# Kernel optimization log

Hardware: AMD Instinct MI355X
Metric: run time of the kernel (lower is better)

## Reference

```python
import jax, jax.numpy as jnp
import numpy as np
import math

# ---- static config (matches init_kwargs) ----
MUL = 16                       # multiplicity of 0e and 1o irreps in/out
IN_DIM = 4 * MUL               # 16x0e + 16x1o -> 16 + 48 = 64 channels
DIAMETER = 7.0
RADIUS = DIAMETER / 2.0
NRB = 8                        # num_radial_basis
STEPS = (1.0, 1.0, 1.0)
N_PATHS = 5                    # 0x0->0, 1x1->0, 0x1->1, 1x0->1, 1x1->1
WEIGHT_NUMEL = N_PATHS * MUL * MUL  # 1280


def _lattice():
    axes = []
    for st in STEPS:
        s = math.floor(RADIUS / st)
        axes.append(np.arange(-s, s + 1.0) * st)
    return np.stack(np.meshgrid(*axes, indexing='ij'), axis=-1).astype(np.float32)  # [kx,ky,kz,3]


def _radial_emb(r):
    # e3nn soft_one_hot_linspace, basis='smooth_finite', cutoff=True
    values = np.linspace(0.0, RADIUS, NRB + 2)[1:-1].astype(np.float32)
    step = values[1] - values[0]
    diff = (r[..., None] - values) / step
    def u(t):  # soft unit step: exp(-1/t) for t>0 else 0
        return np.where(t > 0.0, np.exp(-1.0 / np.where(t > 0.0, t, 1.0)), 0.0)
    return (1.14136 * math.e ** 2 * u(diff + 1.0) * u(1.0 - diff)).astype(np.float32)


def _spherical_harmonics(lat):
    # normalize=True, normalization='component': Y0 = 1, Y1 = sqrt(3) * unit_vec
    n = np.linalg.norm(lat, axis=-1, keepdims=True)
    unit = np.where(n > 0, lat / np.where(n > 0, n, 1.0), 0.0)
    return np.ones(lat.shape[:-1], np.float32), (math.sqrt(3.0) * unit).astype(np.float32)


_LAT = _lattice()
_EMB = jnp.asarray(_radial_emb(np.linalg.norm(_LAT, axis=-1)))  # [kx,ky,kz,NRB]
_sh0_np, _sh1_np = _spherical_harmonics(_LAT)
_SH0, _SH1 = jnp.asarray(_sh0_np), jnp.asarray(_sh1_np)
_eps_np = np.zeros((3, 3, 3), np.float32)
for _i, _j, _k in [(0, 1, 2), (1, 2, 0), (2, 0, 1)]:
    _eps_np[_i, _j, _k] = 1.0
    _eps_np[_i, _k, _j] = -1.0
_EPS = jnp.asarray(_eps_np)


def _build_kernel(tp_weight):
    """Radial-basis matmul + CG tensor-product -> conv kernel [out,in,kx,ky,kz]."""
    kx, ky, kz = _LAT.shape[:3]
    nk = kx * ky * kz
    w = jnp.einsum('xyzb,bn->xyzn', _EMB, tp_weight) / nk
    w = w.reshape(kx, ky, kz, N_PATHS, MUL, MUL)
    w1, w2, w3, w4, w5 = [w[..., p, :, :] for p in range(N_PATHS)]
    # e3nn path weights ('component' norm, 'element' path norm): sqrt(dim_out / fan_in)
    a0 = math.sqrt(1.0 / (2 * MUL))  # -> 0e: paths 1,2 each mul1*mul2 = MUL
    a1 = math.sqrt(3.0 / (3 * MUL))  # -> 1o: paths 3,4,5
    c1 = a0                          # w3j(0,0,0) = 1
    c2 = a0 / math.sqrt(3.0)         # w3j(1,1,0) = delta/sqrt(3)
    c3 = a1 / math.sqrt(3.0)         # w3j(0,1,1) = delta/sqrt(3)
    c4 = a1 / math.sqrt(3.0)         # w3j(1,0,1) = delta/sqrt(3)
    c5 = a1 / math.sqrt(6.0)         # w3j(1,1,1) = eps/sqrt(6)
    Kss = c1 * _SH0[..., None, None] * w1                                  # [k,u,o]
    Kvs = c2 * jnp.einsum('xyzi,xyzuo->xyzuio', _SH1, w2)                  # [k,u,3,o]
    Ksv = c3 * jnp.einsum('xyzk,xyzuo->xyzuok', _SH1, w3)                  # [k,u,o,3]
    eye3 = jnp.eye(3, dtype=w.dtype)
    Kvv = (c4 * jnp.einsum('xyz,ik,xyzuo->xyzuiok', _SH0, eye3, w4)
           + c5 * jnp.einsum('ijk,xyzj,xyzuo->xyzuiok', _EPS, _SH1, w5))   # [k,u,3,o,3]
    top = jnp.concatenate([Kss, Ksv.reshape(kx, ky, kz, MUL, 3 * MUL)], axis=-1)
    bot = jnp.concatenate([Kvs.reshape(kx, ky, kz, 3 * MUL, MUL),
                           Kvv.reshape(kx, ky, kz, 3 * MUL, 3 * MUL)], axis=-1)
    K = jnp.concatenate([top, bot], axis=-2)                               # [kx,ky,kz,in,out]
    return jnp.transpose(K, (4, 3, 0, 1, 2))                               # oixyz


def setup_inputs() -> dict:
    key = jax.random.key(0)
    k1, k2, k3, k4 = jax.random.split(key, 4)
    x = jax.random.normal(k1, (2, IN_DIM, 40, 40, 40), jnp.float32)
    sc_w0 = jax.random.normal(k2, (MUL, MUL), jnp.float32)
    sc_w1 = jax.random.normal(k3, (MUL, MUL), jnp.float32)
    tp_weight = jax.random.normal(k4, (NRB, WEIGHT_NUMEL), jnp.float32)
    return {"x": x, "sc_w0": sc_w0, "sc_w1": sc_w1, "tp_weight": tp_weight}


def reference(x, sc_w0, sc_w1, tp_weight):
    B = x.shape[0]
    sp = x.shape[2:]
    inv = 1.0 / math.sqrt(MUL)  # e3nn Linear fan-in normalization
    x0 = x[:, :MUL]                                  # [B,MUL,D,H,W]
    x1 = x[:, MUL:].reshape(B, MUL, 3, *sp)          # [B,MUL,3,D,H,W]
    sc0 = jnp.einsum('uo,budhw->bodhw', sc_w0, x0) * inv
    sc1 = jnp.einsum('uo,buidhw->boidhw', sc_w1, x1) * inv
    sc = jnp.concatenate([sc0, sc1.reshape(B, 3 * MUL, *sp)], axis=1)
    K = _build_kernel(tp_weight)
    pad = [(s // 2, s // 2) for s in K.shape[2:]]
    conv = jax.lax.conv_general_dilated(
        x, K, window_strides=(1, 1, 1), padding=pad,
        dimension_numbers=('NCDHW', 'OIDHW', 'NCDHW'))
    return sc + conv
```

## Files before the change

### kernel.cpp

```cpp
#include <hip/hip_runtime.h>
#include <stdint.h>


#define NT_REAL 179
#define NT_PAD  180
#define NGRP    45

#define XCH  1557376
#define XCHB ((size_t)XCH * 2)

typedef short s16x8 __attribute__((ext_vector_type(8)));
typedef float f32x4 __attribute__((ext_vector_type(4)));

struct Taps {
  int n;
  short dl16[NT_PAD];
  unsigned char dz[NT_PAD], dy[NT_PAD], dx[NT_PAD];
};
constexpr Taps mk_taps() {
  Taps t{};
  t.n = 0;
  for (int a = 0; a < 7; ++a)
    for (int b = 0; b < 7; ++b)
      for (int c = 0; c < 7; ++c) {
        int d2 = (a-3)*(a-3) + (b-3)*(b-3) + (c-3)*(c-3);
        if (d2 <= 12) {
          t.dz[t.n] = (unsigned char)a; t.dy[t.n] = (unsigned char)b;
          t.dx[t.n] = (unsigned char)c;
          t.dl16[t.n] = (short)((a*14 + b)*16 + c);
          ++t.n;
        }
      }
  for (int i = t.n; i < NT_PAD; ++i) {
    t.dz[i] = 3; t.dy[i] = 3; t.dx[i] = 3; t.dl16[i] = t.dl16[0];
  }
  return t;
}
__device__ constexpr Taps TAPS = mk_taps();
static_assert(mk_taps().n == NT_REAL, "tap count");

struct DL4s { unsigned long long v[NGRP]; };
constexpr DL4s mk_dl4() {
  DL4s d{};
  Taps t = mk_taps();
  for (int g = 0; g < NGRP; ++g) {
    unsigned long long v = 0;
    for (int q = 0; q < 4; ++q)
      v |= (unsigned long long)(unsigned short)t.dl16[g * 4 + q] << (16 * q);
    d.v[g] = v;
  }
  return d;
}
__device__ constexpr DL4s DL4 = mk_dl4();

static __device__ inline unsigned short f2bf(float f) {
  unsigned int u = __float_as_uint(f);
  unsigned int r = u + 0x7FFFu + ((u >> 16) & 1u);
  return (unsigned short)(r >> 16);
}

__device__ __forceinline__ void gl_lds16(const void* g, void* s) {
  __builtin_amdgcn_global_load_lds(
      (const __attribute__((address_space(1))) void*)g,
      (__attribute__((address_space(3))) void*)s, 16, 0, 0);
}

__global__ void prep(const float* __restrict__ x, const float* __restrict__ scw0,
                     const float* __restrict__ scw1, const float* __restrict__ tpw,
                     unsigned short* __restrict__ Xp, unsigned short* __restrict__ Bwp) {
  __shared__ float buf[160 * 65];
  int tid = threadIdx.x;

  if (blockIdx.x < 800) {
    int blk = blockIdx.x;
    int ys = blk % 10; int t2 = blk / 10; int iz = t2 % 40; int b = t2 / 40;
    int y0 = ys * 4;
    const float* src = x + (size_t)b * 4096000 + (size_t)iz * 1600 + (size_t)y0 * 40;
    for (int e = tid; e < 64 * 160; e += 256) {
      int ch = e / 160, i = e - ch * 160;
      buf[i * 65 + ch] = src[(size_t)ch * 64000 + i];
    }
    __syncthreads();
    for (int f = tid; f < 160 * 8; f += 256) {
      int i = f >> 3, g = f & 7;
      int yy = i / 40, xx = i - yy * 40;
      s16x8 v;
      #pragma unroll
      for (int j = 0; j < 8; ++j) v[j] = (short)f2bf(buf[i * 65 + g * 8 + j]);
      size_t pos = ((size_t)((b * 46 + iz + 3) * 46 + (y0 + yy + 3)) * 46 + (xx + 3));
      *reinterpret_cast<s16x8*>(Xp + (size_t)g * XCH + pos * 8) = v;
    }
    return;
  }

  int t = blockIdx.x - 800;
  float (*wsm)[16][16] = reinterpret_cast<float (*)[16][16]>(buf);

  int dz = TAPS.dz[t], dy = TAPS.dy[t], dx = TAPS.dx[t];
  float fz = dz - 3.0f, fy = dy - 3.0f, fx = dx - 3.0f;
  float d2 = fz*fz + fy*fy + fx*fx;
  float r = sqrtf(d2);

  const float step = 3.5f / 9.0f;
  const float Cc = 1.14136f * 7.38905609893065f;
  float emb[8];
  for (int bb = 0; bb < 8; ++bb) {
    float diff = (r - step * (bb + 1)) / step;
    float t1 = diff + 1.0f, t2 = 1.0f - diff;
    float u1 = (t1 > 0.0f) ? expf(-1.0f / t1) : 0.0f;
    float u2 = (t2 > 0.0f) ? expf(-1.0f / t2) : 0.0f;
    emb[bb] = Cc * u1 * u2;
  }

  int u = tid >> 4, o = tid & 15;
  for (int p = 0; p < 5; ++p) {
    float acc = 0.0f;
    int nidx = (p * 16 + u) * 16 + o;
    for (int bb = 0; bb < 8; ++bb) acc += emb[bb] * tpw[bb * 1280 + nidx];
    wsm[p][u][o] = acc * (1.0f / 343.0f);
  }
  __syncthreads();

  float invr = (d2 > 0.0f) ? (1.7320508075688772f / r) : 0.0f;
  float sh[3] = { fz * invr, fy * invr, fx * invr };

  bool center = (dz == 3 && dy == 3 && dx == 3);
  bool padt = (t >= NT_REAL);
  const float c1 = 0.17677669529663687f;
  const float c2 = 0.10206207261596575f;
  const float c3 = 0.14433756729740643f;
  const float c4 = 0.14433756729740643f;
  const float c5 = 0.10206207261596575f;
  const float inv = 0.25f;

  for (int e = tid; e < 4096; e += 256) {
    int ich = e & 63, och = e >> 6;
    float v = 0.0f;
    if (!padt) {
      if (och < 16) {
        if (ich < 16) {
          v = c1 * wsm[0][ich][och];
          if (center) v += inv * scw0[ich * 16 + och];
        } else {
          int qq = ich - 16; int uu = qq / 3, ii = qq % 3;
          v = c2 * sh[ii] * wsm[1][uu][och];
        }
      } else {
        int qo = och - 16; int oo = qo / 3, kk = qo % 3;
        if (ich < 16) {
          v = c3 * sh[kk] * wsm[2][ich][oo];
        } else {
          int qi = ich - 16; int uu = qi / 3, ii = qi % 3;
          if (ii == kk) {
            v = c4 * wsm[3][uu][oo];
            if (center) v += inv * scw1[uu * 16 + oo];
          } else {
            int jj = 3 - ii - kk;
            float sgn = (((kk - ii + 3) % 3) == 2) ? 1.0f : -1.0f;
            v = c5 * sgn * sh[jj] * wsm[4][uu][oo];
          }
        }
      }
    }
    int chunk = ich >> 3, j = ich & 7, q = t & 3, grp = t >> 2;
    int nt = och >> 4, n = och & 15;
    size_t idx = (((((size_t)chunk * NGRP + grp) * 4 + nt) * 4 + q) * 16 + n) * 8 + j;
    Bwp[idx] = f2bf(v);
  }
}

__global__ __launch_bounds__(256, 2) void conv3d(
    const unsigned short* __restrict__ Xp,
    const unsigned short* __restrict__ Bwp,
    float* __restrict__ out) {
  __shared__ __align__(16) unsigned char smem[76800];
  unsigned char* XH = smem;
  unsigned char* BB = smem + 35840;

  int blk = blockIdx.x;
  int p = ((blk & 7) << 6) | (blk >> 3);
  if (p >= 500) return;
  int b = p / 250; int rem = p - b * 250;
  int tz = rem / 25, ty = (rem / 5) % 5, tx = rem % 5;

  int tid = threadIdx.x;
  int lane = tid & 63;
  int w = tid >> 6;
  int q = lane >> 4, n = lane & 15;
  int qs = q << 4;

  size_t hbase = (size_t)(((b * 46 + tz * 4) * 46 + ty * 8) * 46 + tx * 8) * 16;

  int abase = w * 224 + ((n >> 3) << 4) + (n & 7);

  f32x4 acc[4][4];
  #pragma unroll
  for (int a = 0; a < 4; ++a)
    #pragma unroll
    for (int nt = 0; nt < 4; ++nt) acc[a][nt] = f32x4{0.f, 0.f, 0.f, 0.f};

  auto stageB = [&](int c, int s, unsigned char* dst) {
    const unsigned char* bg = (const unsigned char*)Bwp
        + ((size_t)c * NGRP + s * 5) * 4096;
    for (int k = w; k < 20; k += 4)
      gl_lds16(bg + (k << 10) + lane * 16, dst + (k << 10));
  };
  auto stageH = [&](int c) {
    const unsigned char* xc = (const unsigned char*)Xp + (size_t)c * XCHB + hbase;
    for (int k = w; k < 35; k += 4) {
      int sl = (k << 6) + lane;
      int hx = sl & 15; hx = hx > 13 ? 13 : hx;
      int r = sl >> 4;
      int hz = (r * 2341) >> 15;
      int hy = r - hz * 14;
      gl_lds16(xc + ((size_t)((hz * 46 + hy) * 46 + hx)) * 16, XH + (k << 10));
    }
  };

  stageB(0, 0, BB);

  int t = 0;
  for (int c = 0; c < 8; ++c) {
    stageH(c);
    __syncthreads();
    for (int s = 0; s < 9; ++s, ++t) {
      if (t + 1 < 72) {
        int cn = (s == 8) ? c + 1 : c;
        int sn = (s == 8) ? 0 : s + 1;
        stageB(cn, sn, BB + ((t + 1) & 1) * 20480);
      }
      const unsigned char* BSc = BB + (t & 1) * 20480 + (size_t)lane * 16;
      #pragma unroll
      for (int gg = 0; gg < 5; ++gg) {
        unsigned long long dlv = DL4.v[s * 5 + gg];
        int dl = (int)((dlv >> qs) & 0xFFFFull);
        const unsigned char* ab = XH + ((size_t)(abase + dl) << 4);
        s16x8 a0 = *(const s16x8*)(ab);
        s16x8 a1 = *(const s16x8*)(ab + 512);
        s16x8 a2 = *(const s16x8*)(ab + 1024);
        s16x8 a3 = *(const s16x8*)(ab + 1536);
        const unsigned char* bp = BSc + (gg << 12);
        s16x8 b0 = *(const s16x8*)(bp);
        s16x8 b1 = *(const s16x8*)(bp + 1024);
        s16x8 b2 = *(const s16x8*)(bp + 2048);
        s16x8 b3 = *(const s16x8*)(bp + 3072);
        acc[0][0] = __builtin_amdgcn_mfma_f32_16x16x32_bf16(a0, b0, acc[0][0], 0, 0, 0);
        acc[0][1] = __builtin_amdgcn_mfma_f32_16x16x32_bf16(a0, b1, acc[0][1], 0, 0, 0);
        acc[0][2] = __builtin_amdgcn_mfma_f32_16x16x32_bf16(a0, b2, acc[0][2], 0, 0, 0);
        acc[0][3] = __builtin_amdgcn_mfma_f32_16x16x32_bf16(a0, b3, acc[0][3], 0, 0, 0);
        acc[1][0] = __builtin_amdgcn_mfma_f32_16x16x32_bf16(a1, b0, acc[1][0], 0, 0, 0);
        acc[1][1] = __builtin_amdgcn_mfma_f32_16x16x32_bf16(a1, b1, acc[1][1], 0, 0, 0);
        acc[1][2] = __builtin_amdgcn_mfma_f32_16x16x32_bf16(a1, b2, acc[1][2], 0, 0, 0);
        acc[1][3] = __builtin_amdgcn_mfma_f32_16x16x32_bf16(a1, b3, acc[1][3], 0, 0, 0);
        acc[2][0] = __builtin_amdgcn_mfma_f32_16x16x32_bf16(a2, b0, acc[2][0], 0, 0, 0);
        acc[2][1] = __builtin_amdgcn_mfma_f32_16x16x32_bf16(a2, b1, acc[2][1], 0, 0, 0);
        acc[2][2] = __builtin_amdgcn_mfma_f32_16x16x32_bf16(a2, b2, acc[2][2], 0, 0, 0);
        acc[2][3] = __builtin_amdgcn_mfma_f32_16x16x32_bf16(a2, b3, acc[2][3], 0, 0, 0);
        acc[3][0] = __builtin_amdgcn_mfma_f32_16x16x32_bf16(a3, b0, acc[3][0], 0, 0, 0);
        acc[3][1] = __builtin_amdgcn_mfma_f32_16x16x32_bf16(a3, b1, acc[3][1], 0, 0, 0);
        acc[3][2] = __builtin_amdgcn_mfma_f32_16x16x32_bf16(a3, b2, acc[3][2], 0, 0, 0);
        acc[3][3] = __builtin_amdgcn_mfma_f32_16x16x32_bf16(a3, b3, acc[3][3], 0, 0, 0);
      }
      __syncthreads();
    }
  }

  #pragma unroll
  for (int nt = 0; nt < 4; ++nt) {
    size_t cb = (size_t)(b * 64 + nt * 16 + n) * 64000
              + (size_t)(tz * 4 + w) * 1600
              + (size_t)(tx * 8 + (q & 1) * 4);
    #pragma unroll
    for (int a = 0; a < 4; ++a) {
      float* dst = out + cb + (size_t)(ty * 8 + a * 2 + (q >> 1)) * 40;
      *reinterpret_cast<f32x4*>(dst) = acc[a][nt];
    }
  }
}

extern "C" void kernel_launch(void* const* d_in, const int* in_sizes, int n_in,
                              void* d_out, int out_size, void* d_ws, size_t ws_size,
                              hipStream_t stream) {
  const float* x    = (const float*)d_in[0];
  const float* scw0 = (const float*)d_in[1];
  const float* scw1 = (const float*)d_in[2];
  const float* tpw  = (const float*)d_in[3];
  float* out = (float*)d_out;

  unsigned short* Xp  = (unsigned short*)d_ws;
  unsigned short* Bwp = Xp + (size_t)8 * XCH;

  hipMemsetAsync(Xp, 0, (size_t)8 * XCH * 2, stream);
  prep<<<800 + NT_PAD, 256, 0, stream>>>(x, scw0, scw1, tpw, Xp, Bwp);
  conv3d<<<512, 256, 0, stream>>>(Xp, Bwp, out);
}
```

Measured before the change: 236.2 us.

## Switch conv to 32x32x16 MFMA with larger z-tiles and double-buffered halo

```diff
diff --git a/kernel.cpp b/kernel.cpp
--- a/kernel.cpp
+++ b/kernel.cpp
@@ -4,13 +4,18 @@
 
 #define NT_REAL 179
 #define NT_PAD  180
-#define NGRP    45
+#define NPAIR   90
 
 #define XCH  1557376
 #define XCHB ((size_t)XCH * 2)
 
+#define HBYTES 50176
+#define SEGB   12288
+#define NSEG   15
+
 typedef short s16x8 __attribute__((ext_vector_type(8)));
 typedef float f32x4 __attribute__((ext_vector_type(4)));
+typedef float f32x16 __attribute__((ext_vector_type(16)));
 
 struct Taps {
   int n;
@@ -39,19 +44,16 @@
 __device__ constexpr Taps TAPS = mk_taps();
 static_assert(mk_taps().n == NT_REAL, "tap count");
 
-struct DL4s { unsigned long long v[NGRP]; };
-constexpr DL4s mk_dl4() {
-  DL4s d{};
+struct DL2 { unsigned int v[NPAIR]; };
+constexpr DL2 mk_dl2() {
+  DL2 d{};
   Taps t = mk_taps();
-  for (int g = 0; g < NGRP; ++g) {
-    unsigned long long v = 0;
-    for (int q = 0; q < 4; ++q)
-      v |= (unsigned long long)(unsigned short)t.dl16[g * 4 + q] << (16 * q);
-    d.v[g] = v;
-  }
+  for (int p = 0; p < NPAIR; ++p)
+    d.v[p] = (unsigned int)(unsigned short)t.dl16[2*p]
+           | ((unsigned int)(unsigned short)t.dl16[2*p + 1] << 16);
   return d;
 }
-__device__ constexpr DL4s DL4 = mk_dl4();
+__device__ constexpr DL2 DL2V = mk_dl2();
 
 static __device__ inline unsigned short f2bf(float f) {
   unsigned int u = __float_as_uint(f);
@@ -162,118 +164,122 @@
         }
       }
     }
-    int chunk = ich >> 3, j = ich & 7, q = t & 3, grp = t >> 2;
-    int nt = och >> 4, n = och & 15;
-    size_t idx = (((((size_t)chunk * NGRP + grp) * 4 + nt) * 4 + q) * 16 + n) * 8 + j;
+    int chunk = ich >> 3, j = ich & 7;
+    int pair = t >> 1, hi = t & 1;
+    int og = och >> 5, col = och & 31;
+    size_t idx = ((((size_t)chunk * NPAIR + pair) * 2 + og) * 2 + hi) * 256
+               + (size_t)col * 8 + j;
     Bwp[idx] = f2bf(v);
   }
 }
 
-__global__ __launch_bounds__(256, 2) void conv3d(
+__global__ __launch_bounds__(256, 1) void conv3d(
     const unsigned short* __restrict__ Xp,
     const unsigned short* __restrict__ Bwp,
     float* __restrict__ out) {
-  __shared__ __align__(16) unsigned char smem[76800];
-  unsigned char* XH = smem;
-  unsigned char* BB = smem + 35840;
+  __shared__ __align__(16) unsigned char smem[2 * HBYTES + 2 * SEGB];
+  unsigned char* BB = smem + 2 * HBYTES;
 
   int blk = blockIdx.x;
-  int p = ((blk & 7) << 6) | (blk >> 3);
-  if (p >= 500) return;
-  int b = p / 250; int rem = p - b * 250;
+  int p = ((blk & 7) << 5) | (blk >> 3);
+  if (p >= 250) return;
+  int b = p / 125; int rem = p - b * 125;
   int tz = rem / 25, ty = (rem / 5) % 5, tx = rem % 5;
 
   int tid = threadIdx.x;
   int lane = tid & 63;
   int w = tid >> 6;
-  int q = lane >> 4, n = lane & 15;
-  int qs = q << 4;
-
-  size_t hbase = (size_t)(((b * 46 + tz * 4) * 46 + ty * 8) * 46 + tx * 8) * 16;
-
-  int abase = w * 224 + ((n >> 3) << 4) + (n & 7);
-
-  f32x4 acc[4][4];
+  int hi = lane >> 5, r32 = lane & 31;
+  int hs = hi << 4;
+
+  size_t hbase = (size_t)(((b * 46 + tz * 8) * 46 + ty * 8) * 46 + tx * 8) * 16;
+
+  int abase = w * 448 + ((r32 >> 3) << 4) + (r32 & 7);
+
+  f32x16 acc[4][2];
   #pragma unroll
-  for (int a = 0; a < 4; ++a)
+  for (int f = 0; f < 4; ++f)
     #pragma unroll
-    for (int nt = 0; nt < 4; ++nt) acc[a][nt] = f32x4{0.f, 0.f, 0.f, 0.f};
-
-  auto stageB = [&](int c, int s, unsigned char* dst) {
+    for (int og = 0; og < 2; ++og)
+      #pragma unroll
+      for (int e = 0; e < 16; ++e) acc[f][og][e] = 0.0f;
+
+  auto stageB = [&](int c, int seg, unsigned char* dst) {
     const unsigned char* bg = (const unsigned char*)Bwp
-        + ((size_t)c * NGRP + s * 5) * 4096;
-    for (int k = w; k < 20; k += 4)
+        + ((size_t)c * NPAIR + seg * 6) * 2048;
+    for (int k = w; k < 12; k += 4)
       gl_lds16(bg + (k << 10) + lane * 16, dst + (k << 10));
   };
-  auto stageH = [&](int c) {
+  auto stageHLine = [&](int c, int k, unsigned char* dst) {
     const unsigned char* xc = (const unsigned char*)Xp + (size_t)c * XCHB + hbase;
-    for (int k = w; k < 35; k += 4) {
-      int sl = (k << 6) + lane;
-      int hx = sl & 15; hx = hx > 13 ? 13 : hx;
-      int r = sl >> 4;
-      int hz = (r * 2341) >> 15;
-      int hy = r - hz * 14;
-      gl_lds16(xc + ((size_t)((hz * 46 + hy) * 46 + hx)) * 16, XH + (k << 10));
-    }
+    int sl = (k << 6) + lane;
+    int hx = sl & 15; hx = hx > 13 ? 13 : hx;
+    int r = sl >> 4;
+    int hz = (r * 2341) >> 15;
+    int hy = r - hz * 14;
+    gl_lds16(xc + ((size_t)((hz * 46 + hy) * 46 + hx)) * 16, dst + (k << 10));
   };
 
+  for (int k = w; k < 49; k += 4) stageHLine(0, k, smem);
   stageB(0, 0, BB);
+  __syncthreads();
 
   int t = 0;
   for (int c = 0; c < 8; ++c) {
-    stageH(c);
-    __syncthreads();
-    for (int s = 0; s < 9; ++s, ++t) {
-      if (t + 1 < 72) {
-        int cn = (s == 8) ? c + 1 : c;
-        int sn = (s == 8) ? 0 : s + 1;
-        stageB(cn, sn, BB + ((t + 1) & 1) * 20480);
-      }
-      const unsigned char* BSc = BB + (t & 1) * 20480 + (size_t)lane * 16;
+    unsigned char* XH  = smem + (c & 1) * HBYTES;
+    unsigned char* XHn = smem + ((c + 1) & 1) * HBYTES;
+    for (int s = 0; s < NSEG; ++s, ++t) {
+      if (t + 1 < 120) {
+        int cn = (s == NSEG - 1) ? c + 1 : c;
+        int sn = (s == NSEG - 1) ? 0 : s + 1;
+        stageB(cn, sn, BB + ((t + 1) & 1) * SEGB);
+      }
+      if (c + 1 < 8) {
+        int L = s * 4 + w;
+        if (L < 49) stageHLine(c + 1, L, XHn);
+      }
+      const unsigned char* BSc = BB + (t & 1) * SEGB + (size_t)lane * 16;
       #pragma unroll
-      for (int gg = 0; gg < 5; ++gg) {
-        unsigned long long dlv = DL4.v[s * 5 + gg];
-        int dl = (int)((dlv >> qs) & 0xFFFFull);
+      for (int pp = 0; pp < 6; ++pp) {
+        unsigned int dlv = DL2V.v[s * 6 + pp];
+        int dl = (int)((dlv >> hs) & 0xFFFFu);
         const unsigned char* ab = XH + ((size_t)(abase + dl) << 4);
-        s16x8 a0 = *(const s16x8*)(ab);
-        s16x8 a1 = *(const s16x8*)(ab + 512);
-        s16x8 a2 = *(const s16x8*)(ab + 1024);
-        s16x8 a3 = *(const s16x8*)(ab + 1536);
-        const unsigned char* bp = BSc + (gg << 12);
+        s16x8 a00 = *(const s16x8*)(ab);
+        s16x8 a01 = *(const s16x8*)(ab + 1024);
+        s16x8 a10 = *(const s16x8*)(ab + 3584);
+        s16x8 a11 = *(const s16x8*)(ab + 4608);
+        const unsigned char* bp = BSc + (pp << 11);
         s16x8 b0 = *(const s16x8*)(bp);
         s16x8 b1 = *(const s16x8*)(bp + 1024);
-        s16x8 b2 = *(const s16x8*)(bp + 2048);
-        s16x8 b3 = *(const s16x8*)(bp + 3072);
-        acc[0][0] = __builtin_amdgcn_mfma_f32_16x16x32_bf16(a0, b0, acc[0][0], 0, 0, 0);
-        acc[0][1] = __builtin_amdgcn_mfma_f32_16x16x32_bf16(a0, b1, acc[0][1], 0, 0, 0);
-        acc[0][2] = __builtin_amdgcn_mfma_f32_16x16x32_bf16(a0, b2, acc[0][2], 0, 0, 0);
-        acc[0][3] = __builtin_amdgcn_mfma_f32_16x16x32_bf16(a0, b3, acc[0][3], 0, 0, 0);
-        acc[1][0] = __builtin_amdgcn_mfma_f32_16x16x32_bf16(a1, b0, acc[1][0], 0, 0, 0);
-        acc[1][1] = __builtin_amdgcn_mfma_f32_16x16x32_bf16(a1, b1, acc[1][1], 0, 0, 0);
-        acc[1][2] = __builtin_amdgcn_mfma_f32_16x16x32_bf16(a1, b2, acc[1][2], 0, 0, 0);
-        acc[1][3] = __builtin_amdgcn_mfma_f32_16x16x32_bf16(a1, b3, acc[1][3], 0, 0, 0);
-        acc[2][0] = __builtin_amdgcn_mfma_f32_16x16x32_bf16(a2, b0, acc[2][0], 0, 0, 0);
-        acc[2][1] = __builtin_amdgcn_mfma_f32_16x16x32_bf16(a2, b1, acc[2][1], 0, 0, 0);
-        acc[2][2] = __builtin_amdgcn_mfma_f32_16x16x32_bf16(a2, b2, acc[2][2], 0, 0, 0);
-        acc[2][3] = __builtin_amdgcn_mfma_f32_16x16x32_bf16(a2, b3, acc[2][3], 0, 0, 0);
-        acc[3][0] = __builtin_amdgcn_mfma_f32_16x16x32_bf16(a3, b0, acc[3][0], 0, 0, 0);
-        acc[3][1] = __builtin_amdgcn_mfma_f32_16x16x32_bf16(a3, b1, acc[3][1], 0, 0, 0);
-        acc[3][2] = __builtin_amdgcn_mfma_f32_16x16x32_bf16(a3, b2, acc[3][2], 0, 0, 0);
-        acc[3][3] = __builtin_amdgcn_mfma_f32_16x16x32_bf16(a3, b3, acc[3][3], 0, 0, 0);
+        acc[0][0] = __builtin_amdgcn_mfma_f32_32x32x16_bf16(a00, b0, acc[0][0], 0, 0, 0);
+        acc[0][1] = __builtin_amdgcn_mfma_f32_32x32x16_bf16(a00, b1, acc[0][1], 0, 0, 0);
+        acc[1][0] = __builtin_amdgcn_mfma_f32_32x32x16_bf16(a01, b0, acc[1][0], 0, 0, 0);
+        acc[1][1] = __builtin_amdgcn_mfma_f32_32x32x16_bf16(a01, b1, acc[1][1], 0, 0, 0);
+        acc[2][0] = __builtin_amdgcn_mfma_f32_32x32x16_bf16(a10, b0, acc[2][0], 0, 0, 0);
+        acc[2][1] = __builtin_amdgcn_mfma_f32_32x32x16_bf16(a10, b1, acc[2][1], 0, 0, 0);
+        acc[3][0] = __builtin_amdgcn_mfma_f32_32x32x16_bf16(a11, b0, acc[3][0], 0, 0, 0);
+        acc[3][1] = __builtin_amdgcn_mfma_f32_32x32x16_bf16(a11, b1, acc[3][1], 0, 0, 0);
       }
       __syncthreads();
     }
   }
 
+  int col = lane & 31;
   #pragma unroll
-  for (int nt = 0; nt < 4; ++nt) {
-    size_t cb = (size_t)(b * 64 + nt * 16 + n) * 64000
-              + (size_t)(tz * 4 + w) * 1600
-              + (size_t)(tx * 8 + (q & 1) * 4);
+  for (int og = 0; og < 2; ++og) {
     #pragma unroll
-    for (int a = 0; a < 4; ++a) {
-      float* dst = out + cb + (size_t)(ty * 8 + a * 2 + (q >> 1)) * 40;
-      *reinterpret_cast<f32x4*>(dst) = acc[a][nt];
+    for (int f = 0; f < 4; ++f) {
+      int zz = f >> 1, aq = f & 1;
+      size_t cb = (size_t)(b * 64 + og * 32 + col) * 64000
+                + (size_t)(tz * 8 + 2 * w + zz) * 1600
+                + (size_t)(tx * 8 + hi * 4);
+      #pragma unroll
+      for (int ys = 0; ys < 4; ++ys) {
+        float* dst = out + cb + (size_t)(ty * 8 + aq * 4 + ys) * 40;
+        f32x4 v = { acc[f][og][ys * 4 + 0], acc[f][og][ys * 4 + 1],
+                    acc[f][og][ys * 4 + 2], acc[f][og][ys * 4 + 3] };
+        *reinterpret_cast<f32x4*>(dst) = v;
+      }
     }
   }
 }
@@ -292,5 +298,5 @@
 
   hipMemsetAsync(Xp, 0, (size_t)8 * XCH * 2, stream);
   prep<<<800 + NT_PAD, 256, 0, stream>>>(x, scw0, scw1, tpw, Xp, Bwp);
-  conv3d<<<512, 256, 0, stream>>>(Xp, Bwp, out);
-}
+  conv3d<<<256, 256, 0, stream>>>(Xp, Bwp, out);
+}
```

After: 259.5 us. 1.1x slower.
